# Performance work log

Hardware: AMD Instinct MI355X
Metric: run time of the kernel (lower is better)

Reference implementation:

```python
import jax, jax.numpy as jnp
import numpy as np
from jax import lax

B, Hs, Ws = 2, 256, 256
DIM = 256        # query channels (c)
DIM_BAK = 256    # key/value channels (c2)
HEADS = 8
WIN = 8
HEAD_DIM = DIM // HEADS
SCALE = HEAD_DIM ** -0.5


def window_partition(x, ws):
    # x: [B, H, W, C] -> [B*nH*nW, ws, ws, C]
    b, h, w, c = x.shape
    x = x.reshape(b, h // ws, ws, w // ws, ws, c)
    return x.transpose(0, 1, 3, 2, 4, 5).reshape(-1, ws, ws, c)


def window_reverse(windows, ws, h, w):
    # windows: [B*nH*nW, ws, ws, C] -> [B, H, W, C]
    b = windows.shape[0] // ((h // ws) * (w // ws))
    x = windows.reshape(b, h // ws, w // ws, ws, ws, -1)
    return x.transpose(0, 1, 3, 2, 4, 5).reshape(b, h, w, -1)


def setup_inputs() -> dict:
    key = jax.random.key(0)
    ks = jax.random.split(key, 9)
    s = 0.02
    return {
        "query_feature": jax.random.normal(ks[0], (B, DIM, Hs, Ws), jnp.float32),
        "key_value_feature": jax.random.normal(ks[1], (B, DIM_BAK, Hs, Ws), jnp.float32),
        # depthwise 3x3 conv on kv (groups=DIM_BAK, bias=False): OIHW with I=1
        "w_dw": jax.random.normal(ks[2], (DIM_BAK, 1, 3, 3), jnp.float32) * s,
        # to_q: Linear(dim -> dim), stored [in, out]
        "wq": jax.random.normal(ks[3], (DIM, DIM), jnp.float32) * s,
        "bq": jax.random.normal(ks[4], (DIM,), jnp.float32) * s,
        # to_kv: Linear(dim_bak -> 2*dim)
        "wkv": jax.random.normal(ks[5], (DIM_BAK, 2 * DIM), jnp.float32) * s,
        "bkv": jax.random.normal(ks[6], (2 * DIM,), jnp.float32) * s,
        # project_out: Linear(dim -> dim)
        "w_proj": jax.random.normal(ks[7], (DIM, DIM), jnp.float32) * s,
        "b_proj": jax.random.normal(ks[8], (DIM,), jnp.float32) * s,
    }


def reference(query_feature, key_value_feature, w_dw, wq, bq, wkv, bkv, w_proj, b_proj):
    b, c, h, w = query_feature.shape
    c2 = key_value_feature.shape[1]

    # depthwise 3x3 conv on key/value feature (padding=1, stride=1)
    kv = lax.conv_general_dilated(
        key_value_feature, w_dw,
        window_strides=(1, 1), padding="SAME",
        feature_group_count=c2,
        dimension_numbers=("NCHW", "OIHW", "NCHW"))

    # NCHW -> NHWC, partition into non-overlapping windows
    qw = window_partition(query_feature.transpose(0, 2, 3, 1), WIN)  # [B_, ws, ws, c]
    kvw = window_partition(kv.transpose(0, 2, 3, 1), WIN)            # [B_, ws, ws, c2]
    B_ = qw.shape[0]
    N = WIN * WIN
    qw = qw.reshape(B_, N, c)
    kvw = kvw.reshape(B_, N, c2)

    # projections -> multi-head [B_, heads, N, head_dim]
    q = (qw @ wq + bq).reshape(B_, N, HEADS, HEAD_DIM).transpose(0, 2, 1, 3) * SCALE
    kv_proj = (kvw @ wkv + bkv).reshape(B_, N, 2, HEADS, HEAD_DIM)
    k = kv_proj[:, :, 0].transpose(0, 2, 1, 3)
    v = kv_proj[:, :, 1].transpose(0, 2, 1, 3)

    # windowed cross-attention
    attn = jax.nn.softmax(jnp.einsum("bhnd,bhmd->bhnm", q, k), axis=-1)
    out = jnp.einsum("bhnm,bhmd->bhnd", attn, v)
    out = out.transpose(0, 2, 1, 3).reshape(B_, N, c)
    out = out @ w_proj + b_proj

    # reverse windows, back to NCHW
    out = window_reverse(out.reshape(B_, WIN, WIN, c), WIN, h, w)
    return out.transpose(0, 3, 1, 2)
```

## Files before the change

### kernel.cpp

```cpp
#include <hip/hip_runtime.h>
#include <hip/hip_bf16.h>
#include <cstdint>
#include <cstddef>

typedef __hip_bfloat16 bf16;
typedef short bf16x8 __attribute__((ext_vector_type(8)));
typedef float f32x4 __attribute__((ext_vector_type(4)));

#define MFMA(a, b, c) __builtin_amdgcn_mfma_f32_16x16x32_bf16((a), (b), (c), 0, 0, 0)

__global__ __launch_bounds__(256) void stage_k(
    const float* __restrict__ wq, const float* __restrict__ wkv,
    const float* __restrict__ wp, bf16* __restrict__ wqT,
    bf16* __restrict__ wkvT, bf16* __restrict__ wpT,
    const float* __restrict__ qf, bf16* __restrict__ qwM,
    const float* __restrict__ kvf, bf16* __restrict__ SK,
    int b0, int nb, int skmask, int wbP, int do_w) {
  __shared__ bf16 T[64][66];
  int bid = blockIdx.x;
  int tid = threadIdx.x;
  int wb = do_w ? 1024 : 0;
  if (bid < wb) {
    int idx = bid * 256 + tid;
    if (idx < 65536) {
      int n = idx >> 8, k = idx & 255;
      wqT[idx] = __float2bfloat16(wq[k * 256 + n]);
    } else if (idx < 196608) {
      int i = idx - 65536;
      int n = i >> 8, k = i & 255;
      wkvT[i] = __float2bfloat16(wkv[k * 512 + n]);
    } else {
      int i = idx - 196608;
      int n = i >> 8, k = i & 255;
      wpT[i] = __float2bfloat16(wp[k * 256 + n]);
    }
    return;
  }
  int tile = bid - wb;
  int qtiles = nb * 4096;
  if (tile < qtiles) {
    int b = b0 + (tile >> 12);
    int t = tile & 4095;
    int c0 = (t & 3) << 6;
    int hwb = (t >> 2) << 6;
    const float* src = qf + ((size_t)b << 24);
    {
      int hwl = tid & 63, cb = tid >> 6;
      const float* s = src + (size_t)(c0 + cb) * 65536 + hwb + hwl;
#pragma unroll
      for (int i = 0; i < 16; ++i)
        T[cb + i * 4][hwl] = __float2bfloat16(s[(size_t)i * 4 * 65536]);
    }
    __syncthreads();
    {
      int cl = tid & 63, hb = tid >> 6;
      int swoff = b * 1024 - wbP;
#pragma unroll
      for (int j = 0; j < 16; ++j) {
        int hwl = hb + j * 4;
        int hw = hwb + hwl;
        int h = hw >> 8, w = hw & 255;
        int sw = swoff + ((h >> 3) << 5) + (w >> 3);
        int tt = ((h & 7) << 3) + (w & 7);
        qwM[((size_t)(sw * 64 + tt) << 8) + c0 + cl] = T[cl][hwl];
      }
    }
  } else {
    tile -= qtiles;
    int b = b0 + (tile >> 12);
    int t = tile & 4095;
    int c0 = (t & 3) << 6;
    int hwoff = (t >> 2) << 6;
    const float* src = kvf + ((size_t)b << 24);
    bf16* dst = SK + (size_t)(b & skmask) * 16777216;
    {
      int hwl = tid & 63, cb = tid >> 6;
      const float* s = src + (size_t)(c0 + cb) * 65536 + hwoff + hwl;
#pragma unroll
      for (int i = 0; i < 16; ++i)
        T[cb + i * 4][hwl] = __float2bfloat16(s[(size_t)i * 4 * 65536]);
    }
    __syncthreads();
    {
      int cl = tid & 63, hb = tid >> 6;
#pragma unroll
      for (int j = 0; j < 16; ++j) {
        int hwl = hb + j * 4;
        dst[((size_t)(hwoff + hwl) << 8) + c0 + cl] = T[cl][hwl];
      }
    }
  }
}

__global__ __launch_bounds__(256) void wtrans_k(const float* __restrict__ wq,
                                                const float* __restrict__ wkv,
                                                const float* __restrict__ wp,
                                                bf16* __restrict__ wqT,
                                                bf16* __restrict__ wkvT,
                                                bf16* __restrict__ wpT) {
  int idx = blockIdx.x * 256 + threadIdx.x;
  if (idx < 65536) {
    int n = idx >> 8, k = idx & 255;
    wqT[idx] = __float2bfloat16(wq[k * 256 + n]);
  } else if (idx < 196608) {
    int i = idx - 65536;
    int n = i >> 8, k = i & 255;
    wkvT[i] = __float2bfloat16(wkv[k * 512 + n]);
  } else {
    int i = idx - 196608;
    int n = i >> 8, k = i & 255;
    wpT[i] = __float2bfloat16(wp[k * 256 + n]);
  }
}

__global__ __launch_bounds__(256) void t_winq_k(const float* __restrict__ src,
                                                bf16* __restrict__ dst,
                                                int hw0, int swoff) {
  __shared__ bf16 T[64][66];
  int tile = blockIdx.x;
  int c0 = (tile & 3) << 6;
  int hwb = hw0 + ((tile >> 2) << 6);
  int tid = threadIdx.x;
  {
    int hwl = tid & 63, cb = tid >> 6;
    const float* s = src + (size_t)(c0 + cb) * 65536 + hwb + hwl;
#pragma unroll
    for (int i = 0; i < 16; ++i)
      T[cb + i * 4][hwl] = __float2bfloat16(s[(size_t)i * 4 * 65536]);
  }
  __syncthreads();
  {
    int cl = tid & 63, hb = tid >> 6;
#pragma unroll
    for (int j = 0; j < 16; ++j) {
      int hwl = hb + j * 4;
      int hw = hwb + hwl;
      int h = hw >> 8, w = hw & 255;
      int sw = swoff + ((h >> 3) << 5) + (w >> 3);
      int t = ((h & 7) << 3) + (w & 7);
      dst[((size_t)(sw * 64 + t) << 8) + c0 + cl] = T[cl][hwl];
    }
  }
}

__global__ __launch_bounds__(256) void t_nhwc_k(const float* __restrict__ src,
                                                bf16* __restrict__ dst) {
  __shared__ bf16 T[64][66];
  int tile = blockIdx.x;
  int c0 = (tile & 3) << 6;
  int hwoff = (tile >> 2) << 6;
  int tid = threadIdx.x;
  {
    int hwl = tid & 63, cb = tid >> 6;
    const float* s = src + (size_t)(c0 + cb) * 65536 + hwoff + hwl;
#pragma unroll
    for (int i = 0; i < 16; ++i)
      T[cb + i * 4][hwl] = __float2bfloat16(s[(size_t)i * 4 * 65536]);
  }
  __syncthreads();
  {
    int cl = tid & 63, hb = tid >> 6;
#pragma unroll
    for (int j = 0; j < 16; ++j) {
      int hwl = hb + j * 4;
      dst[((size_t)(hwoff + hwl) << 8) + c0 + cl] = T[cl][hwl];
    }
  }
}

__global__ __launch_bounds__(256) void convkv_k(const bf16* __restrict__ SK,
                                                const float* __restrict__ wdw,
                                                const bf16* __restrict__ wkvT,
                                                const float* __restrict__ bkv,
                                                bf16* __restrict__ k_s,
                                                bf16* __restrict__ vT_s,
                                                int wid_base, int cnt, int psw0,
                                                int skmask) {
  __shared__ __align__(16) bf16 X[64 * 256];
  auto xp = [&](int row, int col) -> bf16* {
    int by = (row << 9) + (col << 1);
    by ^= (row & 7) << 4;
    return (bf16*)((char*)X + by);
  };
  int bid = blockIdx.x;
  int swc = (bid & 7) * (cnt >> 3) + (bid >> 3);
  int sw = psw0 + swc;
  int wid = wid_base + swc;
  int b = wid >> 10;
  int rem = wid & 1023, wh = rem >> 5, ww = rem & 31;
  int h0 = wh * 8, w0 = ww * 8;
  const bf16* SKb = SK + (size_t)(b & skmask) * 16777216;
  int tid = threadIdx.x;
  {
    int tg = tid >> 7;
    int cg = tid & 127;
    float wr0[9], wr1[9];
#pragma unroll
    for (int q = 0; q < 9; ++q) {
      wr0[q] = wdw[(cg * 2) * 9 + q];
      wr1[q] = wdw[(cg * 2 + 1) * 9 + q];
    }
    const bool wlo = (w0 > 0), whi = (w0 < 248);
    float rows[3][10][2];
    auto load_row = [&](int gh, float (*r)[2]) {
      if (gh >= 0 && gh < 256) {
        const bf16* rp = SKb + ((size_t)(gh * 256 + w0) << 8) + cg * 2;
        auto up = [&](int off, float* d) {
          uint32_t v = *(const uint32_t*)&rp[off];
          d[0] = __uint_as_float(v << 16);
          d[1] = __uint_as_float(v & 0xffff0000u);
        };
        if (wlo) up(-256, r[0]); else { r[0][0] = 0.f; r[0][1] = 0.f; }
#pragma unroll
        for (int s = 1; s <= 8; ++s) up((s - 1) * 256, r[s]);
        if (whi) up(8 * 256, r[9]); else { r[9][0] = 0.f; r[9][1] = 0.f; }
      } else {
#pragma unroll
        for (int e = 0; e < 10; ++e) { r[e][0] = 0.f; r[e][1] = 0.f; }
      }
    };
    int hb = h0 + tg * 4;
    load_row(hb - 1, rows[0]);
    load_row(hb, rows[1]);
#pragma unroll
    for (int ir = 0; ir < 4; ++ir) {
      load_row(hb + ir + 1, rows[(ir + 2) % 3]);
#pragma unroll
      for (int j = 0; j < 8; ++j) {
        float a0 = 0.f, a1 = 0.f;
#pragma unroll
        for (int di = 0; di < 3; ++di) {
          const float(*rp)[2] = rows[(ir + di) % 3];
#pragma unroll
          for (int dj = 0; dj < 3; ++dj) {
            a0 = __builtin_fmaf(wr0[di * 3 + dj], rp[j + dj][0], a0);
            a1 = __builtin_fmaf(wr1[di * 3 + dj], rp[j + dj][1], a1);
          }
        }
        bf16* p = xp((tg * 4 + ir) * 8 + j, cg * 2);
        p[0] = __float2bfloat16(a0);
        p[1] = __float2bfloat16(a1);
      }
    }
  }
  __syncthreads();
  int wave = tid >> 6, lane = tid & 63, quad = lane >> 4, l16 = lane & 15;
  int n0 = wave * 64;
  f32x4 zero4 = {0.f, 0.f, 0.f, 0.f};
  f32x4 acc[4][4];
  for (int mt = 0; mt < 4; ++mt)
    for (int nt = 0; nt < 4; ++nt) acc[mt][nt] = zero4;
  for (int k0 = 0; k0 < 256; k0 += 32) {
    bf16x8 a[4], bb[4];
    for (int mt = 0; mt < 4; ++mt)
      a[mt] = *(const bf16x8*)xp(mt * 16 + l16, k0 + quad * 8);
    for (int nt = 0; nt < 4; ++nt)
      bb[nt] = *(const bf16x8*)&wkvT[(size_t)(n0 + nt * 16 + l16) * 256 + k0 + quad * 8];
    for (int mt = 0; mt < 4; ++mt)
      for (int nt = 0; nt < 4; ++nt) acc[mt][nt] = MFMA(a[mt], bb[nt], acc[mt][nt]);
  }
  for (int nt = 0; nt < 4; ++nt) {
    int n = n0 + nt * 16 + l16;
    float bias = bkv[n];
    for (int mt = 0; mt < 4; ++mt) {
      int mb = mt * 16 + quad * 4;
      for (int r = 0; r < 4; ++r)
        k_s[((size_t)(sw * 64 + mb + r) << 8) + n] =
            __float2bfloat16(acc[mt][nt][r] + bias);
    }
  }
  for (int mt = 0; mt < 4; ++mt)
    for (int nt = 0; nt < 4; ++nt) acc[mt][nt] = zero4;
  for (int k0 = 0; k0 < 256; k0 += 32) {
    bf16x8 a[4], bb[4];
    for (int mt = 0; mt < 4; ++mt)
      a[mt] = *(const bf16x8*)xp(mt * 16 + l16, k0 + quad * 8);
    for (int nt = 0; nt < 4; ++nt)
      bb[nt] = *(const bf16x8*)&wkvT[(size_t)(256 + n0 + nt * 16 + l16) * 256 + k0 + quad * 8];
    for (int mt = 0; mt < 4; ++mt)
      for (int nt = 0; nt < 4; ++nt) acc[mt][nt] = MFMA(bb[nt], a[mt], acc[mt][nt]);
  }
  for (int nt = 0; nt < 4; ++nt) {
    for (int r = 0; r < 4; ++r) {
      int vd = n0 + nt * 16 + quad * 4 + r;
      float bias = bkv[256 + vd];
      for (int mt = 0; mt < 4; ++mt)
        vT_s[((size_t)(sw * 256 + vd) << 6) + mt * 16 + l16] =
            __float2bfloat16(acc[mt][nt][r] + bias);
    }
  }
}

__global__ __launch_bounds__(256, 2) void fused_k(const bf16* __restrict__ qwM,
                                                  const bf16* __restrict__ wqT,
                                                  const float* __restrict__ bq,
                                                  const bf16* __restrict__ k_s,
                                                  const bf16* __restrict__ vT_s,
                                                  const bf16* __restrict__ wpT,
                                                  const float* __restrict__ bp,
                                                  float* __restrict__ out,
                                                  int wid_base, int nw) {
  __shared__ __align__(16) bf16 XQ[64 * 256];
  int bid = blockIdx.x;
  int sw = (bid & 7) * (nw >> 3) + (bid >> 3);
  int wid = wid_base + sw;
  int b = wid >> 10, rem = wid & 1023, wh = rem >> 5, ww = rem & 31;
  int h0 = wh * 8, w0 = ww * 8;
  int tid = threadIdx.x, wave = tid >> 6, lane = tid & 63, quad = lane >> 4, l16 = lane & 15;
  const bf16* kw = k_s + ((size_t)sw << 14);
  const bf16* vw = vT_s + ((size_t)sw << 14);

  {
    const char* Aq = (const char*)(qwM + ((size_t)sw << 14));
#pragma unroll
    for (int rr = 0; rr < 8; ++rr) {
      int L = rr * 4096 + wave * 1024 + lane * 16;
      int gl = L ^ (((L >> 9) & 7) << 4);
      __builtin_amdgcn_global_load_lds(
          (const __attribute__((address_space(1))) void*)(Aq + gl),
          (__attribute__((address_space(3))) void*)((char*)XQ + rr * 4096 + wave * 1024),
          16, 0, 0);
    }
  }
  bf16x8 kfrA[4];
  {
    int co = wave * 32;
#pragma unroll
    for (int nt = 0; nt < 4; ++nt)
      kfrA[nt] = *(const bf16x8*)&kw[(size_t)(nt * 16 + l16) * 256 + co + quad * 8];
  }
  __syncthreads();

  auto xq = [&](int row, int col) -> const bf16* {
    int by = (row << 9) + (col << 1);
    by ^= (row & 7) << 4;
    return (const bf16*)((const char*)XQ + by);
  };
  char* Abase = (char*)XQ + wave * 8192;
  auto ap = [&](int row, int col) -> bf16* {
    int by = (row << 7) + (col << 1);
    by ^= (row & 7) << 4;
    return (bf16*)(Abase + by);
  };
  auto apR = [&](int w, int row, int col) -> bf16* {
    int by = (row << 7) + (col << 1);
    by ^= (row & 7) << 4;
    return (bf16*)((char*)XQ + w * 8192 + by);
  };
  f32x4 zero4 = {0.f, 0.f, 0.f, 0.f};

  f32x4 qacc[4][4];
  for (int mt = 0; mt < 4; ++mt)
    for (int nt = 0; nt < 4; ++nt) qacc[mt][nt] = zero4;
  for (int k0 = 0; k0 < 256; k0 += 32) {
    bf16x8 a[4], bb[4];
    for (int mt = 0; mt < 4; ++mt)
      a[mt] = *(const bf16x8*)xq(mt * 16 + l16, k0 + quad * 8);
    for (int nt = 0; nt < 4; ++nt) {
      int n = (wave + ((nt >> 1) << 2)) * 32 + (nt & 1) * 16 + l16;
      bb[nt] = *(const bf16x8*)&wqT[(size_t)n * 256 + k0 + quad * 8];
    }
    for (int mt = 0; mt < 4; ++mt)
      for (int nt = 0; nt < 4; ++nt) qacc[mt][nt] = MFMA(a[mt], bb[nt], qacc[mt][nt]);
  }
  __syncthreads();
  {
    const float scale = 0.1767766952966369f;
    for (int nt = 0; nt < 4; ++nt) {
      int n = (wave + ((nt >> 1) << 2)) * 32 + (nt & 1) * 16 + l16;
      float bias = bq[n];
      for (int mt = 0; mt < 4; ++mt) {
        int mb = mt * 16 + quad * 4;
        for (int r = 0; r < 4; ++r)
          *ap(mb + r, nt * 16 + l16) =
              __float2bfloat16((qacc[mt][nt][r] + bias) * scale);
      }
    }
  }
#pragma unroll
  for (int hi = 0; hi < 2; ++hi) {
    int co = (wave + hi * 4) * 32;
    int lc = hi * 32;
    f32x4 s[4][4];
    for (int mt = 0; mt < 4; ++mt)
      for (int nt = 0; nt < 4; ++nt) s[mt][nt] = zero4;
    {
      bf16x8 a[4];
      for (int mt = 0; mt < 4; ++mt)
        a[mt] = *(const bf16x8*)ap(mt * 16 + l16, lc + quad * 8);
      __builtin_amdgcn_s_setprio(1);
      for (int mt = 0; mt < 4; ++mt)
#pragma unroll
        for (int nt = 0; nt < 4; ++nt) s[mt][nt] = MFMA(a[mt], kfrA[nt], s[mt][nt]);
      __builtin_amdgcn_s_setprio(0);
    }
    bf16x8 vb[2][2];
#pragma unroll
    for (int half = 0; half < 2; ++half)
#pragma unroll
      for (int nt = 0; nt < 2; ++nt)
        vb[half][nt] =
            *(const bf16x8*)&vw[(size_t)(co + nt * 16 + l16) * 64 + half * 32 + quad * 8];
    if (hi == 0) {
      int co1 = (wave + 4) * 32;
#pragma unroll
      for (int nt = 0; nt < 4; ++nt)
        kfrA[nt] = *(const bf16x8*)&kw[(size_t)(nt * 16 + l16) * 256 + co1 + quad * 8];
    }
    float rsum[4][4];
    for (int mt = 0; mt < 4; ++mt) {
      for (int r = 0; r < 4; ++r) {
        float m = s[mt][0][r];
        for (int nt = 1; nt < 4; ++nt) m = fmaxf(m, s[mt][nt][r]);
        m = fmaxf(m, __shfl_xor(m, 1, 64));
        m = fmaxf(m, __shfl_xor(m, 2, 64));
        m = fmaxf(m, __shfl_xor(m, 4, 64));
        m = fmaxf(m, __shfl_xor(m, 8, 64));
        float sum = 0.f;
        for (int nt = 0; nt < 4; ++nt) {
          float e = __expf(s[mt][nt][r] - m);
          s[mt][nt][r] = e;
          sum += e;
        }
        sum += __shfl_xor(sum, 1, 64);
        sum += __shfl_xor(sum, 2, 64);
        sum += __shfl_xor(sum, 4, 64);
        sum += __shfl_xor(sum, 8, 64);
        rsum[mt][r] = sum;
      }
    }
    f32x4 o[4][2];
    for (int mt = 0; mt < 4; ++mt)
      for (int nt = 0; nt < 2; ++nt) o[mt][nt] = zero4;
#pragma unroll
    for (int half = 0; half < 2; ++half) {
      for (int mt = 0; mt < 4; ++mt)
#pragma unroll
        for (int nt2 = 0; nt2 < 2; ++nt2)
          for (int r = 0; r < 4; ++r)
            *ap(mt * 16 + quad * 4 + r, lc + nt2 * 16 + l16) =
                __float2bfloat16(s[mt][half * 2 + nt2][r]);
      bf16x8 pa[4];
      for (int mt = 0; mt < 4; ++mt)
        pa[mt] = *(const bf16x8*)ap(mt * 16 + l16, lc + quad * 8);
      __builtin_amdgcn_s_setprio(1);
      for (int mt = 0; mt < 4; ++mt)
#pragma unroll
        for (int nt = 0; nt < 2; ++nt)
          o[mt][nt] = MFMA(pa[mt], vb[half][nt], o[mt][nt]);
      __builtin_amdgcn_s_setprio(0);
    }
    for (int mt = 0; mt < 4; ++mt) {
      int mb = mt * 16 + quad * 4;
      for (int nt = 0; nt < 2; ++nt)
        for (int r = 0; r < 4; ++r)
          *ap(mb + r, lc + nt * 16 + l16) =
              __float2bfloat16(o[mt][nt][r] / rsum[mt][r]);
    }
  }
  __syncthreads();
  {
    int n0 = wave * 64;
    f32x4 acc[4][4];
    for (int mt = 0; mt < 4; ++mt)
      for (int nt = 0; nt < 4; ++nt) acc[mt][nt] = zero4;
    for (int k0 = 0; k0 < 256; k0 += 32) {
      int head = k0 >> 5;
      int rw = head & 3;
      int lc = (head >> 2) * 32;
      bf16x8 a[4], bb[4];
      for (int mt = 0; mt < 4; ++mt)
        a[mt] = *(const bf16x8*)apR(rw, mt * 16 + l16, lc + quad * 8);
      for (int nt = 0; nt < 4; ++nt)
        bb[nt] = *(const bf16x8*)&wpT[(size_t)(n0 + nt * 16 + l16) * 256 + k0 + quad * 8];
      for (int mt = 0; mt < 4; ++mt)
        for (int nt = 0; nt < 4; ++nt) acc[mt][nt] = MFMA(a[mt], bb[nt], acc[mt][nt]);
    }
    for (int nt = 0; nt < 4; ++nt) {
      int n = n0 + nt * 16 + l16;
      float bias = bp[n];
      float* chan = out + ((size_t)(b * 256 + n) << 16);
      for (int mt = 0; mt < 4; ++mt) {
        int row_i = mt * 2 + (quad >> 1);
        int j0 = (quad & 1) * 4;
        f32x4 v4;
        for (int r = 0; r < 4; ++r) v4[r] = acc[mt][nt][r] + bias;
        *(f32x4*)&chan[(size_t)(h0 + row_i) * 256 + w0 + j0] = v4;
      }
    }
  }
}

extern "C" void kernel_launch(void* const* d_in, const int* in_sizes, int n_in,
                              void* d_out, int out_size, void* d_ws, size_t ws_size,
                              hipStream_t stream) {
  const float* qf  = (const float*)d_in[0];
  const float* kvf = (const float*)d_in[1];
  const float* wdw = (const float*)d_in[2];
  const float* wq  = (const float*)d_in[3];
  const float* bq  = (const float*)d_in[4];
  const float* wkv = (const float*)d_in[5];
  const float* bkv = (const float*)d_in[6];
  const float* wp  = (const float*)d_in[7];
  const float* bp  = (const float*)d_in[8];
  float* out = (float*)d_out;

  bf16* wqT  = (bf16*)d_ws;
  bf16* wkvT = wqT + 65536;
  bf16* wpT  = wkvT + 131072;
  bf16* bufs = wpT + 65536;
  const size_t welems = 65536 + 131072 + 65536;
  const size_t skel = (size_t)256 * 256 * 256;

  size_t fitelems = welems + 2 * skel + (size_t)3 * 2048 * 16384;
  if (fitelems * 2 <= ws_size) {
    bf16* SK  = bufs;
    bf16* qwM = SK + 2 * skel;
    bf16* KS  = qwM + (size_t)2048 * 16384;
    bf16* VT  = KS + (size_t)2048 * 16384;
    stage_k<<<1024 + 2 * 4096 * 2, 256, 0, stream>>>(
        wq, wkv, wp, wqT, wkvT, wpT, qf, qwM, kvf, SK,
        0, 2, 1, 0, 1);
    convkv_k<<<2048, 256, 0, stream>>>(SK, wdw, wkvT, bkv, KS, VT,
                                       0, 2048,
                                       0, 1);
    fused_k<<<2048, 256, 0, stream>>>(qwM, wqT, bq, KS, VT, wpT, bp, out,
                                      0, 2048);
    return;
  }

  size_t midelems = welems + skel + (size_t)3 * 1024 * 16384;
  if (midelems * 2 <= ws_size) {
    bf16* SK  = bufs;
    bf16* qwM = SK + skel;
    bf16* KS  = qwM + (size_t)1024 * 16384;
    bf16* VT  = KS + (size_t)1024 * 16384;
    wtrans_k<<<1024, 256, 0, stream>>>(wq, wkv, wp, wqT, wkvT, wpT);
    for (int b = 0; b < 2; ++b) {
      stage_k<<<2 * 4096, 256, 0, stream>>>(
          wq, wkv, wp, wqT, wkvT, wpT, qf, qwM, kvf, SK,
          b, 1, 0, b * 1024, 0);
      convkv_k<<<1024, 256, 0, stream>>>(SK, wdw, wkvT, bkv, KS, VT,
                                         b * 1024, 1024, 0, 0);
      fused_k<<<1024, 256, 0, stream>>>(qwM, wqT, bq, KS, VT, wpT, bp, out,
                                        b * 1024, 1024);
    }
    return;
  }

  int passes = 4;
  while (passes < 32 &&
         (welems + skel + (size_t)3 * (2048 / passes) * 16384) * 2 > ws_size)
    passes <<= 1;
  int nw = 2048 / passes;
  size_t sz = (size_t)nw * 16384;
  bf16* SK  = bufs;
  bf16* qwM = SK + skel;
  bf16* KS  = qwM + sz;
  bf16* VT  = KS + sz;
  wtrans_k<<<1024, 256, 0, stream>>>(wq, wkv, wp, wqT, wkvT, wpT);
  for (int p = 0; p < passes; ++p) {
    int wbP = p * nw;
    int b0 = wbP >> 10, b1 = (wbP + nw - 1) >> 10;
    for (int b = b0; b <= b1; ++b) {
      int s = wbP > b * 1024 ? wbP : b * 1024;
      int e = (wbP + nw) < (b + 1) * 1024 ? (wbP + nw) : (b + 1) * 1024;
      int cnt = e - s;
      int h0 = ((s & 1023) >> 5) * 8;
      t_winq_k<<<cnt * 4, 256, 0, stream>>>(qf + ((size_t)b << 24), qwM,
                                            h0 * 256, b * 1024 - wbP);
      t_nhwc_k<<<4096, 256, 0, stream>>>(kvf + ((size_t)b << 24), SK);
      convkv_k<<<cnt, 256, 0, stream>>>(SK, wdw, wkvT, bkv, KS, VT,
                                        s, cnt, s - wbP, 0);
    }
    fused_k<<<nw, 256, 0, stream>>>(qwM, wqT, bq, KS, VT, wpT, bp, out, wbP, nw);
  }
}
```

Measured before the change: 574.8 us.

## Use one wave per head in fused attention kernel with 512 threads

```diff
diff --git a/kernel.cpp b/kernel.cpp
--- a/kernel.cpp
+++ b/kernel.cpp
@@ -291,16 +291,16 @@
   }
 }
 
-__global__ __launch_bounds__(256, 2) void fused_k(const bf16* __restrict__ qwM,
-                                                  const bf16* __restrict__ wqT,
-                                                  const float* __restrict__ bq,
-                                                  const bf16* __restrict__ k_s,
-                                                  const bf16* __restrict__ vT_s,
-                                                  const bf16* __restrict__ wpT,
-                                                  const float* __restrict__ bp,
-                                                  float* __restrict__ out,
-                                                  int wid_base, int nw) {
-  __shared__ __align__(16) bf16 XQ[64 * 256];
+__global__ __launch_bounds__(512) void fused_k(const bf16* __restrict__ qwM,
+                                               const bf16* __restrict__ wqT,
+                                               const float* __restrict__ bq,
+                                               const bf16* __restrict__ k_s,
+                                               const bf16* __restrict__ vT_s,
+                                               const bf16* __restrict__ wpT,
+                                               const float* __restrict__ bp,
+                                               float* __restrict__ out,
+                                               int wid_base, int nw) {
+  __shared__ __align__(16) bf16 AR[8 * 64 * 40];
   int bid = blockIdx.x;
   int sw = (bid & 7) * (nw >> 3) + (bid >> 3);
   int wid = wid_base + sw;
@@ -309,174 +309,155 @@
   int tid = threadIdx.x, wave = tid >> 6, lane = tid & 63, quad = lane >> 4, l16 = lane & 15;
   const bf16* kw = k_s + ((size_t)sw << 14);
   const bf16* vw = vT_s + ((size_t)sw << 14);
+  int co = wave * 32;
 
   {
     const char* Aq = (const char*)(qwM + ((size_t)sw << 14));
 #pragma unroll
-    for (int rr = 0; rr < 8; ++rr) {
-      int L = rr * 4096 + wave * 1024 + lane * 16;
+    for (int rr = 0; rr < 4; ++rr) {
+      int L = rr * 8192 + wave * 1024 + lane * 16;
       int gl = L ^ (((L >> 9) & 7) << 4);
       __builtin_amdgcn_global_load_lds(
           (const __attribute__((address_space(1))) void*)(Aq + gl),
-          (__attribute__((address_space(3))) void*)((char*)XQ + rr * 4096 + wave * 1024),
+          (__attribute__((address_space(3))) void*)((char*)AR + L),
           16, 0, 0);
     }
   }
-  bf16x8 kfrA[4];
-  {
-    int co = wave * 32;
-#pragma unroll
-    for (int nt = 0; nt < 4; ++nt)
-      kfrA[nt] = *(const bf16x8*)&kw[(size_t)(nt * 16 + l16) * 256 + co + quad * 8];
-  }
+  bf16x8 kfr[4];
+#pragma unroll
+  for (int nt = 0; nt < 4; ++nt)
+    kfr[nt] = *(const bf16x8*)&kw[(size_t)(nt * 16 + l16) * 256 + co + quad * 8];
   __syncthreads();
 
   auto xq = [&](int row, int col) -> const bf16* {
     int by = (row << 9) + (col << 1);
     by ^= (row & 7) << 4;
-    return (const bf16*)((const char*)XQ + by);
+    return (const bf16*)((const char*)AR + by);
   };
-  char* Abase = (char*)XQ + wave * 8192;
-  auto ap = [&](int row, int col) -> bf16* {
-    int by = (row << 7) + (col << 1);
-    by ^= (row & 7) << 4;
-    return (bf16*)(Abase + by);
+  char* rbase = (char*)AR + wave * 5120;
+  auto rp = [&](int row, int col) -> bf16* {
+    return (bf16*)(rbase + row * 80 + col * 2);
   };
-  auto apR = [&](int w, int row, int col) -> bf16* {
-    int by = (row << 7) + (col << 1);
-    by ^= (row & 7) << 4;
-    return (bf16*)((char*)XQ + w * 8192 + by);
+  auto rpR = [&](int w, int row, int col) -> bf16* {
+    return (bf16*)((char*)AR + w * 5120 + row * 80 + col * 2);
   };
   f32x4 zero4 = {0.f, 0.f, 0.f, 0.f};
 
-  f32x4 qacc[4][4];
+  f32x4 qacc[4][2];
   for (int mt = 0; mt < 4; ++mt)
-    for (int nt = 0; nt < 4; ++nt) qacc[mt][nt] = zero4;
+    for (int nt = 0; nt < 2; ++nt) qacc[mt][nt] = zero4;
   for (int k0 = 0; k0 < 256; k0 += 32) {
-    bf16x8 a[4], bb[4];
+    bf16x8 a[4], bb[2];
     for (int mt = 0; mt < 4; ++mt)
       a[mt] = *(const bf16x8*)xq(mt * 16 + l16, k0 + quad * 8);
-    for (int nt = 0; nt < 4; ++nt) {
-      int n = (wave + ((nt >> 1) << 2)) * 32 + (nt & 1) * 16 + l16;
+    for (int nt = 0; nt < 2; ++nt) {
+      int n = co + nt * 16 + l16;
       bb[nt] = *(const bf16x8*)&wqT[(size_t)n * 256 + k0 + quad * 8];
     }
     for (int mt = 0; mt < 4; ++mt)
-      for (int nt = 0; nt < 4; ++nt) qacc[mt][nt] = MFMA(a[mt], bb[nt], qacc[mt][nt]);
+      for (int nt = 0; nt < 2; ++nt) qacc[mt][nt] = MFMA(a[mt], bb[nt], qacc[mt][nt]);
   }
   __syncthreads();
   {
     const float scale = 0.1767766952966369f;
-    for (int nt = 0; nt < 4; ++nt) {
-      int n = (wave + ((nt >> 1) << 2)) * 32 + (nt & 1) * 16 + l16;
+    for (int nt = 0; nt < 2; ++nt) {
+      int n = co + nt * 16 + l16;
       float bias = bq[n];
       for (int mt = 0; mt < 4; ++mt) {
         int mb = mt * 16 + quad * 4;
         for (int r = 0; r < 4; ++r)
-          *ap(mb + r, nt * 16 + l16) =
+          *rp(mb + r, nt * 16 + l16) =
               __float2bfloat16((qacc[mt][nt][r] + bias) * scale);
       }
     }
   }
-#pragma unroll
-  for (int hi = 0; hi < 2; ++hi) {
-    int co = (wave + hi * 4) * 32;
-    int lc = hi * 32;
-    f32x4 s[4][4];
-    for (int mt = 0; mt < 4; ++mt)
-      for (int nt = 0; nt < 4; ++nt) s[mt][nt] = zero4;
-    {
-      bf16x8 a[4];
-      for (int mt = 0; mt < 4; ++mt)
-        a[mt] = *(const bf16x8*)ap(mt * 16 + l16, lc + quad * 8);
-      __builtin_amdgcn_s_setprio(1);
-      for (int mt = 0; mt < 4; ++mt)
-#pragma unroll
-        for (int nt = 0; nt < 4; ++nt) s[mt][nt] = MFMA(a[mt], kfrA[nt], s[mt][nt]);
-      __builtin_amdgcn_s_setprio(0);
-    }
-    bf16x8 vb[2][2];
-#pragma unroll
-    for (int half = 0; half < 2; ++half)
+  f32x4 s[4][4];
+  for (int mt = 0; mt < 4; ++mt)
+    for (int nt = 0; nt < 4; ++nt) s[mt][nt] = zero4;
+  {
+    bf16x8 a[4];
+    for (int mt = 0; mt < 4; ++mt)
+      a[mt] = *(const bf16x8*)rp(mt * 16 + l16, quad * 8);
+    __builtin_amdgcn_s_setprio(1);
+    for (int mt = 0; mt < 4; ++mt)
+#pragma unroll
+      for (int nt = 0; nt < 4; ++nt) s[mt][nt] = MFMA(a[mt], kfr[nt], s[mt][nt]);
+    __builtin_amdgcn_s_setprio(0);
+  }
+  bf16x8 vb[2][2];
+#pragma unroll
+  for (int half = 0; half < 2; ++half)
+#pragma unroll
+    for (int nt = 0; nt < 2; ++nt)
+      vb[half][nt] =
+          *(const bf16x8*)&vw[(size_t)(co + nt * 16 + l16) * 64 + half * 32 + quad * 8];
+  float rsum[4][4];
+  for (int mt = 0; mt < 4; ++mt) {
+    for (int r = 0; r < 4; ++r) {
+      float m = s[mt][0][r];
+      for (int nt = 1; nt < 4; ++nt) m = fmaxf(m, s[mt][nt][r]);
+      m = fmaxf(m, __shfl_xor(m, 1, 64));
+      m = fmaxf(m, __shfl_xor(m, 2, 64));
+      m = fmaxf(m, __shfl_xor(m, 4, 64));
+      m = fmaxf(m, __shfl_xor(m, 8, 64));
+      float sum = 0.f;
+      for (int nt = 0; nt < 4; ++nt) {
+        float e = __expf(s[mt][nt][r] - m);
+        s[mt][nt][r] = e;
+        sum += e;
+      }
+      sum += __shfl_xor(sum, 1, 64);
+      sum += __shfl_xor(sum, 2, 64);
+      sum += __shfl_xor(sum, 4, 64);
+      sum += __shfl_xor(sum, 8, 64);
+      rsum[mt][r] = sum;
+    }
+  }
+  f32x4 o[4][2];
+  for (int mt = 0; mt < 4; ++mt)
+    for (int nt = 0; nt < 2; ++nt) o[mt][nt] = zero4;
+#pragma unroll
+  for (int half = 0; half < 2; ++half) {
+    for (int mt = 0; mt < 4; ++mt)
+#pragma unroll
+      for (int nt2 = 0; nt2 < 2; ++nt2)
+        for (int r = 0; r < 4; ++r)
+          *rp(mt * 16 + quad * 4 + r, nt2 * 16 + l16) =
+              __float2bfloat16(s[mt][half * 2 + nt2][r]);
+    bf16x8 pa[4];
+    for (int mt = 0; mt < 4; ++mt)
+      pa[mt] = *(const bf16x8*)rp(mt * 16 + l16, quad * 8);
+    __builtin_amdgcn_s_setprio(1);
+    for (int mt = 0; mt < 4; ++mt)
 #pragma unroll
       for (int nt = 0; nt < 2; ++nt)
-        vb[half][nt] =
-            *(const bf16x8*)&vw[(size_t)(co + nt * 16 + l16) * 64 + half * 32 + quad * 8];
-    if (hi == 0) {
-      int co1 = (wave + 4) * 32;
-#pragma unroll
-      for (int nt = 0; nt < 4; ++nt)
-        kfrA[nt] = *(const bf16x8*)&kw[(size_t)(nt * 16 + l16) * 256 + co1 + quad * 8];
-    }
-    float rsum[4][4];
-    for (int mt = 0; mt < 4; ++mt) {
-      for (int r = 0; r < 4; ++r) {
-        float m = s[mt][0][r];
-        for (int nt = 1; nt < 4; ++nt) m = fmaxf(m, s[mt][nt][r]);
-        m = fmaxf(m, __shfl_xor(m, 1, 64));
-        m = fmaxf(m, __shfl_xor(m, 2, 64));
-        m = fmaxf(m, __shfl_xor(m, 4, 64));
-        m = fmaxf(m, __shfl_xor(m, 8, 64));
-        float sum = 0.f;
-        for (int nt = 0; nt < 4; ++nt) {
-          float e = __expf(s[mt][nt][r] - m);
-          s[mt][nt][r] = e;
-          sum += e;
-        }
-        sum += __shfl_xor(sum, 1, 64);
-        sum += __shfl_xor(sum, 2, 64);
-        sum += __shfl_xor(sum, 4, 64);
-        sum += __shfl_xor(sum, 8, 64);
-        rsum[mt][r] = sum;
-      }
-    }
-    f32x4 o[4][2];
-    for (int mt = 0; mt < 4; ++mt)
-      for (int nt = 0; nt < 2; ++nt) o[mt][nt] = zero4;
-#pragma unroll
-    for (int half = 0; half < 2; ++half) {
-      for (int mt = 0; mt < 4; ++mt)
-#pragma unroll
-        for (int nt2 = 0; nt2 < 2; ++nt2)
-          for (int r = 0; r < 4; ++r)
-            *ap(mt * 16 + quad * 4 + r, lc + nt2 * 16 + l16) =
-                __float2bfloat16(s[mt][half * 2 + nt2][r]);
-      bf16x8 pa[4];
-      for (int mt = 0; mt < 4; ++mt)
-        pa[mt] = *(const bf16x8*)ap(mt * 16 + l16, lc + quad * 8);
-      __builtin_amdgcn_s_setprio(1);
-      for (int mt = 0; mt < 4; ++mt)
-#pragma unroll
-        for (int nt = 0; nt < 2; ++nt)
-          o[mt][nt] = MFMA(pa[mt], vb[half][nt], o[mt][nt]);
-      __builtin_amdgcn_s_setprio(0);
-    }
-    for (int mt = 0; mt < 4; ++mt) {
-      int mb = mt * 16 + quad * 4;
-      for (int nt = 0; nt < 2; ++nt)
-        for (int r = 0; r < 4; ++r)
-          *ap(mb + r, lc + nt * 16 + l16) =
-              __float2bfloat16(o[mt][nt][r] / rsum[mt][r]);
-    }
+        o[mt][nt] = MFMA(pa[mt], vb[half][nt], o[mt][nt]);
+    __builtin_amdgcn_s_setprio(0);
+  }
+  for (int mt = 0; mt < 4; ++mt) {
+    int mb = mt * 16 + quad * 4;
+    for (int nt = 0; nt < 2; ++nt)
+      for (int r = 0; r < 4; ++r)
+        *rp(mb + r, nt * 16 + l16) =
+            __float2bfloat16(o[mt][nt][r] / rsum[mt][r]);
   }
   __syncthreads();
   {
-    int n0 = wave * 64;
-    f32x4 acc[4][4];
-    for (int mt = 0; mt < 4; ++mt)
-      for (int nt = 0; nt < 4; ++nt) acc[mt][nt] = zero4;
+    int n0 = wave * 32;
+    f32x4 acc[4][2];
+    for (int mt = 0; mt < 4; ++mt)
+      for (int nt = 0; nt < 2; ++nt) acc[mt][nt] = zero4;
     for (int k0 = 0; k0 < 256; k0 += 32) {
       int head = k0 >> 5;
-      int rw = head & 3;
-      int lc = (head >> 2) * 32;
-      bf16x8 a[4], bb[4];
+      bf16x8 a[4], bb[2];
       for (int mt = 0; mt < 4; ++mt)
-        a[mt] = *(const bf16x8*)apR(rw, mt * 16 + l16, lc + quad * 8);
-      for (int nt = 0; nt < 4; ++nt)
+        a[mt] = *(const bf16x8*)rpR(head, mt * 16 + l16, quad * 8);
+      for (int nt = 0; nt < 2; ++nt)
         bb[nt] = *(const bf16x8*)&wpT[(size_t)(n0 + nt * 16 + l16) * 256 + k0 + quad * 8];
       for (int mt = 0; mt < 4; ++mt)
-        for (int nt = 0; nt < 4; ++nt) acc[mt][nt] = MFMA(a[mt], bb[nt], acc[mt][nt]);
-    }
-    for (int nt = 0; nt < 4; ++nt) {
+        for (int nt = 0; nt < 2; ++nt) acc[mt][nt] = MFMA(a[mt], bb[nt], acc[mt][nt]);
+    }
+    for (int nt = 0; nt < 2; ++nt) {
       int n = n0 + nt * 16 + l16;
       float bias = bp[n];
       float* chan = out + ((size_t)(b * 256 + n) << 16);
@@ -524,7 +505,7 @@
     convkv_k<<<2048, 256, 0, stream>>>(SK, wdw, wkvT, bkv, KS, VT,
                                        0, 2048,
                                        0, 1);
-    fused_k<<<2048, 256, 0, stream>>>(qwM, wqT, bq, KS, VT, wpT, bp, out,
+    fused_k<<<2048, 512, 0, stream>>>(qwM, wqT, bq, KS, VT, wpT, bp, out,
                                       0, 2048);
     return;
   }
@@ -542,7 +523,7 @@
           b, 1, 0, b * 1024, 0);
       convkv_k<<<1024, 256, 0, stream>>>(SK, wdw, wkvT, bkv, KS, VT,
                                          b * 1024, 1024, 0, 0);
-      fused_k<<<1024, 256, 0, stream>>>(qwM, wqT, bq, KS, VT, wpT, bp, out,
+      fused_k<<<1024, 512, 0, stream>>>(qwM, wqT, bq, KS, VT, wpT, bp, out,
                                         b * 1024, 1024);
     }
     return;
@@ -573,6 +554,6 @@
       convkv_k<<<cnt, 256, 0, stream>>>(SK, wdw, wkvT, bkv, KS, VT,
                                         s, cnt, s - wbP, 0);
     }
-    fused_k<<<nw, 256, 0, stream>>>(qwM, wqT, bq, KS, VT, wpT, bp, out, wbP, nw);
-  }
-}
+    fused_k<<<nw, 512, 0, stream>>>(qwM, wqT, bq, KS, VT, wpT, bp, out, wbP, nw);
+  }
+}
```

New measurement: 601.4 us. 1.05x slower.
